# Kernel tuning notes

Measured on AMD Instinct MI355X. Metric: run time of the kernel, lower is better.

The kernel has to match this reference:

```python
import jax, jax.numpy as jnp
import numpy as np

N_NODES, C, R, L, H, NB = 50000, 512, 4096, 32, 4, 4  # NB blocks: enc0, enc1, pma, dec0
LN_EPS = 1e-5

def _layer_norm(x, g, b):
    mu = jnp.mean(x, axis=-1, keepdims=True)
    var = jnp.var(x, axis=-1, keepdims=True)
    return (x - mu) * jax.lax.rsqrt(var + LN_EPS) * g + b

def _mab(x, y, y_mask, x_mask, Wq, bq, Wk, bk, Wv, bv, Wo, bo, ffW, ffb, g1, b1, g2, b2):
    # Multihead attention block (SetTransformer MAB), dropout=0 at inference.
    Rr, Lq, Cc = x.shape
    Lk = y.shape[1]
    Dh = Cc // H
    q = (x @ Wq.T + bq).reshape(Rr, Lq, H, Dh)
    k = (y @ Wk.T + bk).reshape(Rr, Lk, H, Dh)
    v = (y @ Wv.T + bv).reshape(Rr, Lk, H, Dh)
    scores = jnp.einsum('rqhd,rkhd->rhqk', q, k) * (1.0 / Dh ** 0.5)
    if y_mask is not None:  # mask padded keys (ragged gene sets)
        scores = jnp.where(y_mask[:, None, None, :], scores, jnp.float32(-1e30))
    attn = jax.nn.softmax(scores, axis=-1)
    out = jnp.einsum('rhqk,rkhd->rqhd', attn, v).reshape(Rr, Lq, Cc)
    out = out @ Wo.T + bo
    if x_mask is not None:  # zero attention output at padded query rows
        out = jnp.where(x_mask[..., None], out, 0.0)
    out = _layer_norm(out + x, g1, b1)
    out = _layer_norm(out + jax.nn.relu(out @ ffW.T + ffb), g2, b2)
    return out

def setup_inputs() -> dict:
    key = jax.random.key(0)
    ks = jax.random.split(key, 10)
    s = 0.02
    return {
        'gene_embeddings': jax.random.normal(ks[0], (N_NODES, C), jnp.float32),
        'reaction_gene_idx': jax.random.randint(ks[1], (R, L), 0, N_NODES),
        'reaction_lengths': jax.random.randint(ks[2], (R,), 1, L + 1),
        'Wq': jax.random.normal(ks[3], (NB, C, C), jnp.float32) * s,
        'Wk': jax.random.normal(ks[4], (NB, C, C), jnp.float32) * s,
        'Wv': jax.random.normal(ks[5], (NB, C, C), jnp.float32) * s,
        'Wo': jax.random.normal(ks[6], (NB, C, C), jnp.float32) * s,
        'ffW': jax.random.normal(ks[7], (NB, C, C), jnp.float32) * s,
        'bq': jnp.zeros((NB, C), jnp.float32),
        'bk': jnp.zeros((NB, C), jnp.float32),
        'bv': jnp.zeros((NB, C), jnp.float32),
        'bo': jnp.zeros((NB, C), jnp.float32),
        'ffb': jnp.zeros((NB, C), jnp.float32),
        'g1': jnp.ones((NB, C), jnp.float32),
        'b1': jnp.zeros((NB, C), jnp.float32),
        'g2': jnp.ones((NB, C), jnp.float32),
        'b2': jnp.zeros((NB, C), jnp.float32),
        'pma_lin_W': jax.random.normal(ks[8], (C, C), jnp.float32) * s,
        'pma_lin_b': jnp.zeros((C,), jnp.float32),
        'seed': jax.random.normal(ks[9], (1, C), jnp.float32) * s,
    }

def reference(gene_embeddings, reaction_gene_idx, reaction_lengths, Wq, Wk, Wv, Wo, ffW, bq, bk, bv, bo, ffb, g1, b1, g2, b2, pma_lin_W, pma_lin_b, seed):
    mask = jnp.arange(L)[None, :] < reaction_lengths[:, None]  # [R, L] ragged validity mask
    x = gene_embeddings[reaction_gene_idx]                     # [R, L, C] per-reaction gather
    x = jnp.where(mask[..., None], x, 0.0)
    def blk(i, xq, ykv, ymask, xmask):
        return _mab(xq, ykv, ymask, xmask, Wq[i], bq[i], Wk[i], bk[i], Wv[i], bv[i],
                    Wo[i], bo[i], ffW[i], ffb[i], g1[i], b1[i], g2[i], b2[i])
    x = blk(0, x, x, mask, mask)   # encoder SAB 0
    x = blk(1, x, x, mask, mask)   # encoder SAB 1
    y = jax.nn.relu(x @ pma_lin_W.T + pma_lin_b)
    sd = jnp.broadcast_to(seed[None, :, :], (R, 1, C))
    x = blk(2, sd, y, mask, None)  # PMA: 1 seed attends over gene set
    x = blk(3, x, x, None, None)   # decoder SAB over the single seed
    out = jnp.mean(x, axis=1)      # [R, C] (1 seed, concat=False)
    out = jnp.where((reaction_lengths > 0)[:, None], out, 0.0)  # empty reactions -> zeros
    return out
```

## Files before the change

kernel.cpp:

```cpp
#include <hip/hip_runtime.h>
#include <stdint.h>

#define R_ 4096
#define L_ 32
#define C_ 512
#define H_ 4
#define DH_ 128

typedef __bf16 bf16x8 __attribute__((ext_vector_type(8)));
typedef float f32x4 __attribute__((ext_vector_type(4)));

__device__ __forceinline__ float b2f(unsigned int u) {
    union { unsigned int i; float f; } x; x.i = u << 16; return x.f;
}
__device__ __forceinline__ unsigned short f2b(float f) {
    union { float f; unsigned int i; } x; x.f = f;
    unsigned int i = x.i;
    i += 0x7fffu + ((i >> 16) & 1u);
    return (unsigned short)(i >> 16);
}
__device__ __forceinline__ void unpack8(uint4 v, float* x) {
    x[0] = b2f(v.x & 0xffffu); x[1] = b2f(v.x >> 16);
    x[2] = b2f(v.y & 0xffffu); x[3] = b2f(v.y >> 16);
    x[4] = b2f(v.z & 0xffffu); x[5] = b2f(v.z >> 16);
    x[6] = b2f(v.w & 0xffffu); x[7] = b2f(v.w >> 16);
}
__device__ __forceinline__ uint4 pack8(const float* x) {
    uint4 v;
    v.x = (unsigned)f2b(x[0]) | ((unsigned)f2b(x[1]) << 16);
    v.y = (unsigned)f2b(x[2]) | ((unsigned)f2b(x[3]) << 16);
    v.z = (unsigned)f2b(x[4]) | ((unsigned)f2b(x[5]) << 16);
    v.w = (unsigned)f2b(x[6]) | ((unsigned)f2b(x[7]) << 16);
    return v;
}

__device__ __forceinline__ void gload_lds16(const unsigned short* g, unsigned short* l) {
    __builtin_amdgcn_global_load_lds(
        (const __attribute__((address_space(1))) void*)g,
        (__attribute__((address_space(3))) void*)l, 16, 0, 0);
}

__global__ __launch_bounds__(256)
void detect_kernel(const unsigned short* __restrict__ gene, int* __restrict__ flag) {
    __shared__ int cnt;
    if (threadIdx.x == 0) cnt = 0;
    __syncthreads();
    int local = 0;
    for (int j = 0; j < 8; ++j) {
        int i = threadIdx.x * 8 + j;
        unsigned short u = gene[2 * i];
        int e = (u >> 7) & 0xFF;
        if (e >= 100 && e <= 140) ++local;
    }
    atomicAdd(&cnt, local);
    __syncthreads();
    if (threadIdx.x == 0) *flag = (cnt >= 1024) ? 1 : 0;
}

__global__ __launch_bounds__(256)
void cvt_any_kernel(const void* __restrict__ in, unsigned short* __restrict__ out,
                    int n, const int* __restrict__ flag, int src_off) {
    int i0 = (blockIdx.x * 256 + threadIdx.x) * 8;
    if (i0 >= n) return;
    if (*flag) {
        *(uint4*)(out + i0) = *(const uint4*)((const unsigned short*)in + src_off + i0);
    } else {
        const float* f = (const float*)in + src_off;
        float4 a = *(const float4*)(f + i0);
        float4 b = *(const float4*)(f + i0 + 4);
        float x[8] = {a.x, a.y, a.z, a.w, b.x, b.y, b.z, b.w};
        *(uint4*)(out + i0) = pack8(x);
    }
}

__global__ __launch_bounds__(256)
void bias_concat_kernel(const unsigned short* __restrict__ bq, const unsigned short* __restrict__ bk,
                        const unsigned short* __restrict__ bv,
                        unsigned short* __restrict__ bqkv0, unsigned short* __restrict__ bqkv1,
                        unsigned short* __restrict__ bkv2) {
    int t = threadIdx.x;
#pragma unroll
    for (int s = 0; s < 2; ++s) {
        int i = t + s * 256;
        bqkv0[i]        = bq[i];
        bqkv0[i + 512]  = bk[i];
        bqkv0[i + 1024] = bv[i];
        bqkv1[i]        = bq[i + 512];
        bqkv1[i + 512]  = bk[i + 512];
        bqkv1[i + 1024] = bv[i + 512];
        bkv2[i]         = bk[i + 1024];
        bkv2[i + 512]   = bv[i + 1024];
    }
}

__global__ __launch_bounds__(256)
void qp_kernel(const unsigned short* __restrict__ Wq2, const unsigned short* __restrict__ bq2,
               const unsigned short* __restrict__ seed, unsigned short* __restrict__ qp) {
    __shared__ float sv[512];
    int t = threadIdx.x;
    sv[t] = b2f(seed[t]); sv[t + 256] = b2f(seed[t + 256]);
    __syncthreads();
#pragma unroll
    for (int s = 0; s < 2; ++s) {
        int n = t + s * 256;
        const unsigned short* wrow = Wq2 + (size_t)n * 512;
        float acc = 0.f;
        for (int k8 = 0; k8 < 64; ++k8) {
            float x[8];
            unpack8(*(const uint4*)(wrow + k8 * 8), x);
#pragma unroll
            for (int e = 0; e < 8; ++e) acc += x[e] * sv[k8 * 8 + e];
        }
        qp[n] = f2b(acc + b2f(bq2[n]));
    }
}

__global__ __launch_bounds__(256)
void diag_kernel(unsigned short* __restrict__ out, int n, float val) {
    int i = blockIdx.x * 256 + threadIdx.x;
    if (i < n) out[i] = f2b(val);
}

__global__ __launch_bounds__(256)
void scan_kernel(const int* __restrict__ lens, int* __restrict__ off,
                 int* __restrict__ meta, int Rc) {
    __shared__ int tsum[257];
    const int t = threadIdx.x;
    const int chunk = (Rc + 255) / 256;
    const int lo = t * chunk;
    const int hi = min(lo + chunk, Rc);
    int s = 0;
    for (int i = lo; i < hi; ++i) {
        int l = lens[i]; l = max(0, min(32, l));
        s += l;
    }
    tsum[t] = s;
    __syncthreads();
    if (t == 0) {
        int acc = 0;
        for (int i = 0; i < 256; ++i) { int v = tsum[i]; tsum[i] = acc; acc += v; }
        tsum[256] = acc;
        meta[0] = acc;
        meta[1] = (acc + 127) & ~127;
    }
    __syncthreads();
    int run = tsum[t];
    for (int i = lo; i < hi; ++i) {
        off[i] = run;
        int l = lens[i]; l = max(0, min(32, l));
        run += l;
    }
}

__global__ __launch_bounds__(256)
void gather_kernel(const void* __restrict__ gene_v, const int* __restrict__ gidx,
                   const int* __restrict__ lens, const int* __restrict__ off,
                   unsigned short* __restrict__ X, const int* __restrict__ flag) {
    int tid = blockIdx.x * 256 + threadIdx.x;
    int m = tid >> 6;
    int ch = tid & 63;
    int r = m >> 5, j = m & 31;
    if (j >= lens[r]) return;
    size_t dst = (size_t)(off[r] + j) * C_ + ch * 8;
    size_t base = (size_t)gidx[m] * C_ + ch * 8;
    uint4 v;
    if (*flag) {
        v = *(const uint4*)((const unsigned short*)gene_v + base);
    } else {
        const float* f = (const float*)gene_v;
        float4 a = *(const float4*)(f + base);
        float4 b = *(const float4*)(f + base + 4);
        float x[8] = {a.x, a.y, a.z, a.w, b.x, b.y, b.z, b.w};
        v = pack8(x);
    }
    *(uint4*)(X + dst) = v;
}

__global__ __launch_bounds__(256)
void ztail_kernel(unsigned short* __restrict__ X, const int* __restrict__ meta) {
    int tid = blockIdx.x * 256 + threadIdx.x;
    int m = meta[0] + (tid >> 6);
    int ch = tid & 63;
    if (m < meta[1])
        *(uint4*)(X + (size_t)m * C_ + ch * 8) = make_uint4(0u, 0u, 0u, 0u);
}

__global__ __launch_bounds__(256)
void seed_kernel(const unsigned short* __restrict__ seed, unsigned short* __restrict__ Xs) {
    int i = blockIdx.x * 256 + threadIdx.x;
    int ch = i & 63;
    uint4 v = *(const uint4*)(seed + ch * 8);
    *(uint4*)(Xs + (size_t)i * 8) = v;
}

__global__ __launch_bounds__(256)
void final_kernel(const unsigned short* __restrict__ S, const int* __restrict__ lens,
                  void* __restrict__ out, const int* __restrict__ flag, size_t elem_off) {
    int i = blockIdx.x * 256 + threadIdx.x;
    int r = i >> 6;
    uint4 v = make_uint4(0u, 0u, 0u, 0u);
    if (lens[r] > 0) v = *(const uint4*)(S + (size_t)i * 8);
    if (*flag) {
        *(uint4*)((unsigned short*)out + elem_off + (size_t)i * 8) = v;
    } else {
        float x[8];
        unpack8(v, x);
        float* o = (float*)out + elem_off + (size_t)i * 8;
        *(float4*)o       = make_float4(x[0], x[1], x[2], x[3]);
        *(float4*)(o + 4) = make_float4(x[4], x[5], x[6], x[7]);
    }
}

template<int NT>
__global__ __launch_bounds__(256, 2)
void gemm_bt_kernel(const unsigned short* __restrict__ A, const unsigned short* __restrict__ W,
                    const unsigned short* __restrict__ bias, unsigned short* __restrict__ Out,
                    int relu, const int* __restrict__ meta, int MT) {
    const int b = blockIdx.x;
    const int xcd = b & 7;
    const int j = b >> 3;
    const int ml = j / NT;
    const int n = j - ml * NT;
    const int m = ml * 8 + xcd;
    if (m >= MT) return;
    const int m0 = m * 128, n0 = n * 256;
    if (meta && m0 >= meta[1]) return;
    const int ldo = NT * 256;

    __shared__ unsigned short As[128 * 64];
    __shared__ unsigned short Bs[256 * 64];

    const int t = threadIdx.x;
    const int wave = t >> 6, lane = t & 63;
    const int quad = lane >> 4, lr = lane & 15;
    const int wr = wave >> 1, wc = wave & 1;

    const int srow8 = lane >> 3;
    const int scol8 = (lane & 7) ^ srow8;
    const unsigned short* gaB = A + (size_t)(m0 + wave * 8 + srow8) * C_ + scol8 * 8;
    const unsigned short* gbB = W + (size_t)(n0 + wave * 8 + srow8) * C_ + scol8 * 8;
    unsigned short* lA = As + wave * 512;
    unsigned short* lB = Bs + wave * 512;

    f32x4 acc[4][8] = {};

    for (int k0 = 0; k0 < C_; k0 += 64) {
        __syncthreads();
#pragma unroll
        for (int jj = 0; jj < 4; ++jj)
            gload_lds16(gaB + (size_t)jj * 32 * C_ + k0, lA + jj * 2048);
#pragma unroll
        for (int jj = 0; jj < 8; ++jj)
            gload_lds16(gbB + (size_t)jj * 32 * C_ + k0, lB + jj * 2048);
        __syncthreads();

#pragma unroll
        for (int kk = 0; kk < 2; ++kk) {
            bf16x8 af[4], bfr[8];
#pragma unroll
            for (int i = 0; i < 4; ++i)
                af[i] = *(const bf16x8*)&As[(64 * wr + 16 * i + lr) * 64 +
                                            (((kk << 2) + quad) ^ (lr & 7)) * 8];
#pragma unroll
            for (int jj = 0; jj < 8; ++jj)
                bfr[jj] = *(const bf16x8*)&Bs[(128 * wc + 16 * jj + lr) * 64 +
                                              (((kk << 2) + quad) ^ (lr & 7)) * 8];
#pragma unroll
            for (int i = 0; i < 4; ++i)
#pragma unroll
                for (int jj = 0; jj < 8; ++jj)
                    acc[i][jj] = __builtin_amdgcn_mfma_f32_16x16x32_bf16(af[i], bfr[jj], acc[i][jj], 0, 0, 0);
        }
    }

#pragma unroll
    for (int i = 0; i < 4; ++i) {
        int row = m0 + 64 * wr + 16 * i + quad * 4;
#pragma unroll
        for (int jj = 0; jj < 8; ++jj) {
            int col = n0 + 128 * wc + 16 * jj + lr;
            float bv = b2f(bias[col]);
#pragma unroll
            for (int r = 0; r < 4; ++r) {
                float v = acc[i][jj][r] + bv;
                if (relu) v = fmaxf(v, 0.f);
                Out[(size_t)(row + r) * ldo + col] = f2b(v);
            }
        }
    }
}

template<int NK>
__device__ __forceinline__ void attn_enc_body(
    const unsigned short* __restrict__ QKV, unsigned short* __restrict__ O,
    int h, int t, int len, int base,
    unsigned short* Qs, unsigned short* Ks, float (*Sc)[33]) {

#pragma unroll
    for (int it = 0; it < NK; ++it) {
        int flat = t + it * 128;
        int row = flat >> 4, ch = flat & 15;
        if (row < len) {
            size_t g = ((size_t)(base + row)) * 1536 + h * DH_ + ch * 8;
            *(uint4*)&Qs[row * 136 + ch * 8] = *(const uint4*)(QKV + g);
            *(uint4*)&Ks[row * 136 + ch * 8] = *(const uint4*)(QKV + g + 512);
        }
    }
    __syncthreads();

    const unsigned* Qw = (const unsigned*)Qs;
    const unsigned* Kw = (const unsigned*)Ks;

    {
        const int qg = t >> 3, kg = t & 7;
        float aqk[2][NK];
#pragma unroll
        for (int j = 0; j < 2; ++j)
#pragma unroll
            for (int i = 0; i < NK; ++i) aqk[j][i] = 0.f;
        for (int d2 = 0; d2 < 64; ++d2) {
            unsigned q0 = Qw[qg * 68 + d2];
            unsigned q1 = Qw[(qg + 16) * 68 + d2];
            float q0l = b2f(q0 & 0xffffu), q0h = b2f(q0 >> 16);
            float q1l = b2f(q1 & 0xffffu), q1h = b2f(q1 >> 16);
#pragma unroll
            for (int i = 0; i < NK; ++i) {
                unsigned kv = Kw[(kg + 8 * i) * 68 + d2];
                float kl = b2f(kv & 0xffffu), kh = b2f(kv >> 16);
                aqk[0][i] += q0l * kl + q0h * kh;
                aqk[1][i] += q1l * kl + q1h * kh;
            }
        }
        const float scale = 0.08838834764831845f;
#pragma unroll
        for (int j = 0; j < 2; ++j)
#pragma unroll
            for (int i = 0; i < NK; ++i) {
                int k = kg + 8 * i;
                Sc[qg + 16 * j][k] = (k < len) ? aqk[j][i] * scale : -1e30f;
            }
    }
    __syncthreads();

    if (t < len) {
        float mx = -3e38f;
        for (int k = 0; k < len; ++k) mx = fmaxf(mx, Sc[t][k]);
        float sum = 0.f;
        for (int k = 0; k < len; ++k) { float e = __expf(Sc[t][k] - mx); Sc[t][k] = e; sum += e; }
        float inv = 1.f / sum;
        for (int k = 0; k < len; ++k) Sc[t][k] *= inv;
    }
    __syncthreads();

    {
        const int qh = t >> 3, g = t & 7;
        float av[2][16] = {};
        const unsigned short* Vg = QKV + (size_t)base * 1536 + 1024 + h * DH_ + g * 8;
        for (int k = 0; k < len; ++k) {
            float a0 = Sc[qh][k], a1 = Sc[qh + 16][k];
            const unsigned short* vrow = Vg + (size_t)k * 1536;
            float v0[8], v1[8];
            unpack8(*(const uint4*)vrow, v0);
            unpack8(*(const uint4*)(vrow + 64), v1);
#pragma unroll
            for (int e = 0; e < 8; ++e) {
                av[0][e]     += a0 * v0[e];
                av[0][8 + e] += a0 * v1[e];
                av[1][e]     += a1 * v0[e];
                av[1][8 + e] += a1 * v1[e];
            }
        }
#pragma unroll
        for (int qi = 0; qi < 2; ++qi) {
            int q = qh + 16 * qi;
            if (q >= len) continue;
            size_t ga = ((size_t)(base + q)) * C_ + h * DH_;
#pragma unroll
            for (int j = 0; j < 2; ++j) {
                float tmp[8];
#pragma unroll
                for (int e = 0; e < 8; ++e) tmp[e] = av[qi][j * 8 + e];
                *(uint4*)(O + ga + g * 8 + 64 * j) = pack8(tmp);
            }
        }
    }
}

__global__ __launch_bounds__(128)
void attn_enc_kernel(const unsigned short* __restrict__ QKV, unsigned short* __restrict__ O,
                     const int* __restrict__ lens, const int* __restrict__ off) {
    const int r = blockIdx.x, h = blockIdx.y, t = threadIdx.x;
    const int len = lens[r];
    if (len <= 0) return;
    const int base = off[r];
    __shared__ unsigned short Qs[32 * 136], Ks[32 * 136];
    __shared__ float Sc[32][33];
    switch ((len + 7) >> 3) {
        case 1:  attn_enc_body<1>(QKV, O, h, t, len, base, Qs, Ks, Sc); break;
        case 2:  attn_enc_body<2>(QKV, O, h, t, len, base, Qs, Ks, Sc); break;
        case 3:  attn_enc_body<3>(QKV, O, h, t, len, base, Qs, Ks, Sc); break;
        default: attn_enc_body<4>(QKV, O, h, t, len, base, Qs, Ks, Sc); break;
    }
}

__global__ __launch_bounds__(64)
void attn_pma_kernel(const unsigned short* __restrict__ qp, const unsigned short* __restrict__ KV,
                     unsigned short* __restrict__ O,
                     const int* __restrict__ lens, const int* __restrict__ off) {
    const int r = blockIdx.x, h = blockIdx.y, t = threadIdx.x;
    const int len = lens[r];
    if (len <= 0) return;
    const int base = off[r];
    __shared__ float qv[128];
    __shared__ float attn[32];
    const size_t qb = (size_t)r * C_ + h * DH_;
    qv[t]      = b2f(qp[h * DH_ + t]);
    qv[t + 64] = b2f(qp[h * DH_ + t + 64]);
    __syncthreads();
    if (t < 32 && t < len) {
        const unsigned short* krow = KV + ((size_t)(base + t)) * 1024 + h * DH_;
        float s = 0.f;
        for (int d = 0; d < 128; ++d) s += qv[d] * b2f(krow[d]);
        attn[t] = s * 0.08838834764831845f;
    }
    __syncthreads();
    if (t == 0) {
        float mx = -3e38f;
        for (int k = 0; k < len; ++k) mx = fmaxf(mx, attn[k]);
        float sum = 0.f;
        for (int k = 0; k < len; ++k) { float e = __expf(attn[k] - mx); attn[k] = e; sum += e; }
        float inv = 1.f / sum;
        for (int k = 0; k < len; ++k) attn[k] *= inv;
    }
    __syncthreads();
    float a0 = 0.f, a1 = 0.f;
    for (int k = 0; k < len; ++k) {
        const unsigned short* vrow = KV + ((size_t)(base + k)) * 1024 + 512 + h * DH_;
        float a = attn[k];
        a0 += a * b2f(vrow[t]);
        a1 += a * b2f(vrow[t + 64]);
    }
    O[qb + t]      = f2b(a0);
    O[qb + t + 64] = f2b(a1);
}

__global__ __launch_bounds__(256)
void ln_kernel(const unsigned short* __restrict__ A, const unsigned short* __restrict__ Res,
               const unsigned short* __restrict__ gamma, const unsigned short* __restrict__ beta,
               unsigned short* __restrict__ out, const int* __restrict__ lens, int use_mask,
               const int* __restrict__ meta) {
    const int m = blockIdx.x * 4 + (threadIdx.x >> 6);
    if (meta && m >= meta[1]) return;
    const int lane = threadIdx.x & 63;
    const bool masked = use_mask && ((m & 31) >= lens[m >> 5]);
    const size_t base = (size_t)m * C_ + lane * 8;
    float xa[8], xr[8], x[8];
    unpack8(*(const uint4*)(A + base), xa);
    unpack8(*(const uint4*)(Res + base), xr);
    float s = 0.f, ss = 0.f;
#pragma unroll
    for (int e = 0; e < 8; ++e) {
        x[e] = (masked ? 0.f : xa[e]) + xr[e];
        s += x[e]; ss += x[e] * x[e];
    }
#pragma unroll
    for (int off = 32; off > 0; off >>= 1) {
        s  += __shfl_down(s, off);
        ss += __shfl_down(ss, off);
    }
    s = __shfl(s, 0); ss = __shfl(ss, 0);
    const float mu = s * (1.f / 512.f);
    const float rinv = rsqrtf(fmaxf(ss * (1.f / 512.f) - mu * mu, 0.f) + 1e-5f);
    float gg[8], bb[8], y[8];
    unpack8(*(const uint4*)(gamma + lane * 8), gg);
    unpack8(*(const uint4*)(beta + lane * 8), bb);
#pragma unroll
    for (int e = 0; e < 8; ++e) y[e] = (x[e] - mu) * rinv * gg[e] + bb[e];
    *(uint4*)(out + base) = pack8(y);
}

extern "C" void kernel_launch(void* const* d_in, const int* in_sizes, int n_in,
                              void* d_out, int out_size, void* d_ws, size_t ws_size,
                              hipStream_t stream) {
    (void)in_sizes; (void)n_in;
    const void* gene = d_in[0];
    const int*  gidx = (const int*)d_in[1];
    const int*  lens = (const int*)d_in[2];

    int* ibase = (int*)d_ws;
    int* flag  = ibase;
    int* meta  = ibase + 2;
    int* d_off = ibase + 8;
    unsigned short* ws0 = (unsigned short*)(ibase + 8 + 4096);
    const size_t hdr_bytes = (size_t)(8 + 4096) * 4;

    size_t off = 0;
    auto take = [&](size_t elems) { unsigned short* p = ws0 + off; off += elems; return p; };
    const size_t CC = (size_t)C_ * C_;
    unsigned short* wEnc0 = take(3 * CC);
    unsigned short* wEnc1 = take(3 * CC);
    unsigned short* wKVp  = take(2 * CC);
    unsigned short* wO  = take(4 * CC);
    unsigned short* wF  = take(4 * CC);
    unsigned short* wP  = take(CC);
    unsigned short* wQp = take(CC);
    unsigned short* wVd = take(CC);
    unsigned short* cbq = take(4 * C_);
    unsigned short* cbk = take(4 * C_);
    unsigned short* cbv = take(4 * C_);
    unsigned short* cbo = take(4 * C_);
    unsigned short* cff = take(4 * C_);
    unsigned short* cg1 = take(4 * C_);
    unsigned short* cb1 = take(4 * C_);
    unsigned short* cg2 = take(4 * C_);
    unsigned short* cb2 = take(4 * C_);
    unsigned short* cpb = take(C_);
    unsigned short* csd = take(C_);
    unsigned short* bqkv0 = take(3 * C_);
    unsigned short* bqkv1 = take(3 * C_);
    unsigned short* bkv2  = take(2 * C_);
    unsigned short* qp    = take(C_);
    const size_t wbytes = hdr_bytes + off * 2;

    const size_t per_r = ((size_t)32 * 2560 + 4 * 512) * 2;
    int Rc = 0;
    const int cands[6] = {4096, 2048, 1024, 512, 256, 128};
    for (int i = 0; i < 6; ++i) {
        size_t need = wbytes + (size_t)cands[i] * per_r;
        if (need <= ws_size) { Rc = cands[i]; break; }
    }
    if (Rc == 0) {
        diag_kernel<<<(out_size + 255) / 256, 256, 0, stream>>>(
            (unsigned short*)d_out, out_size, 1000.0f + (float)(ws_size >> 20));
        return;
    }
    const int Mc = Rc * 32;

    unsigned short* X    = take((size_t)Mc * C_);
    unsigned short* AQKV = take((size_t)Mc * 1536);
    unsigned short* Aout = take((size_t)Mc * C_);
    unsigned short* S0 = take((size_t)Rc * C_);
    unsigned short* S1 = take((size_t)Rc * C_);
    unsigned short* S2 = take((size_t)Rc * C_);
    unsigned short* S3 = take((size_t)Rc * C_);

    detect_kernel<<<1, 256, 0, stream>>>((const unsigned short*)gene, flag);
    auto cvt = [&](const void* in, unsigned short* out_, int n, int src_off) {
        cvt_any_kernel<<<(n + 2047) / 2048, 256, 0, stream>>>(in, out_, n, flag, src_off);
    };
    cvt(d_in[3], wEnc0,          (int)CC, 0);
    cvt(d_in[4], wEnc0 + CC,     (int)CC, 0);
    cvt(d_in[5], wEnc0 + 2 * CC, (int)CC, 0);
    cvt(d_in[3], wEnc1,          (int)CC, (int)CC);
    cvt(d_in[4], wEnc1 + CC,     (int)CC, (int)CC);
    cvt(d_in[5], wEnc1 + 2 * CC, (int)CC, (int)CC);
    cvt(d_in[4], wKVp,      (int)CC, (int)(2 * CC));
    cvt(d_in[5], wKVp + CC, (int)CC, (int)(2 * CC));
    cvt(d_in[3], wQp, (int)CC, (int)(2 * CC));
    cvt(d_in[5], wVd, (int)CC, (int)(3 * CC));
    cvt(d_in[6], wO, (int)(4 * CC), 0);
    cvt(d_in[7], wF, (int)(4 * CC), 0);
    cvt(d_in[17], wP, (int)CC, 0);
    cvt(d_in[8],  cbq, 4 * C_, 0); cvt(d_in[9],  cbk, 4 * C_, 0); cvt(d_in[10], cbv, 4 * C_, 0);
    cvt(d_in[11], cbo, 4 * C_, 0); cvt(d_in[12], cff, 4 * C_, 0);
    cvt(d_in[13], cg1, 4 * C_, 0); cvt(d_in[14], cb1, 4 * C_, 0);
    cvt(d_in[15], cg2, 4 * C_, 0); cvt(d_in[16], cb2, 4 * C_, 0);
    cvt(d_in[18], cpb, C_, 0);     cvt(d_in[19], csd, C_, 0);
    bias_concat_kernel<<<1, 256, 0, stream>>>(cbq, cbk, cbv, bqkv0, bqkv1, bkv2);
    qp_kernel<<<1, 256, 0, stream>>>(wQp, cbq + 2 * C_, csd, qp);

    auto gemm = [&](auto nt_tag, const unsigned short* Ain, const unsigned short* Win,
                    const unsigned short* bias, unsigned short* Outp, int Mrows, int relu,
                    const int* mt) {
        constexpr int NT = decltype(nt_tag)::value;
        const int MT = Mrows / 128;
        const int grid = 8 * ((MT + 7) / 8) * NT;
        gemm_bt_kernel<NT><<<dim3(grid), 256, 0, stream>>>(Ain, Win, bias, Outp, relu, mt, MT);
    };
    using N2 = std::integral_constant<int, 2>;
    using N4 = std::integral_constant<int, 4>;
    using N6 = std::integral_constant<int, 6>;

    for (int c = 0; c < R_ / Rc; ++c) {
        const int r0 = c * Rc;
        const int* lc = lens + r0;

        scan_kernel<<<1, 256, 0, stream>>>(lc, d_off, meta, Rc);
        gather_kernel<<<Mc * 64 / 256, 256, 0, stream>>>(
            gene, gidx + (size_t)r0 * L_, lc, d_off, X, flag);
        ztail_kernel<<<32, 256, 0, stream>>>(X, meta);

        for (int i = 0; i < 2; ++i) {
            gemm(N6{}, X, i ? wEnc1 : wEnc0, i ? bqkv1 : bqkv0, AQKV, Mc, 0, meta);
            attn_enc_kernel<<<dim3(Rc, H_), 128, 0, stream>>>(AQKV, Aout, lc, d_off);
            gemm(N2{}, Aout, wO + (size_t)i * CC, cbo + i * C_, AQKV, Mc, 0, meta);
            ln_kernel<<<Mc / 4, 256, 0, stream>>>(AQKV, X, cg1 + i * C_, cb1 + i * C_, X, lc, 0, meta);
            gemm(N2{}, X, wF + (size_t)i * CC, cff + i * C_, Aout, Mc, 1, meta);
            ln_kernel<<<Mc / 4, 256, 0, stream>>>(Aout, X, cg2 + i * C_, cb2 + i * C_, X, lc, 0, meta);
        }

        gemm(N2{}, X, wP, cpb, Aout, Mc, 1, meta);
        seed_kernel<<<Rc * 64 / 256, 256, 0, stream>>>(csd, S0);

        {
            gemm(N4{}, Aout, wKVp, bkv2, AQKV, Mc, 0, meta);
            attn_pma_kernel<<<dim3(Rc, H_), 64, 0, stream>>>(qp, AQKV, S2, lc, d_off);
            gemm(N2{}, S2, wO + 2 * CC, cbo + 2 * C_, S3, Rc, 0, nullptr);
            ln_kernel<<<Rc / 4, 256, 0, stream>>>(S3, S0, cg1 + 2 * C_, cb1 + 2 * C_, S0, lc, 0, nullptr);
            gemm(N2{}, S0, wF + 2 * CC, cff + 2 * C_, S1, Rc, 1, nullptr);
            ln_kernel<<<Rc / 4, 256, 0, stream>>>(S1, S0, cg2 + 2 * C_, cb2 + 2 * C_, S0, lc, 0, nullptr);
        }

        {
            gemm(N2{}, S0, wVd, cbv + 3 * C_, S1, Rc, 0, nullptr);
            gemm(N2{}, S1, wO + 3 * CC, cbo + 3 * C_, S2, Rc, 0, nullptr);
            ln_kernel<<<Rc / 4, 256, 0, stream>>>(S2, S0, cg1 + 3 * C_, cb1 + 3 * C_, S0, lc, 0, nullptr);
            gemm(N2{}, S0, wF + 3 * CC, cff + 3 * C_, S1, Rc, 1, nullptr);
            ln_kernel<<<Rc / 4, 256, 0, stream>>>(S1, S0, cg2 + 3 * C_, cb2 + 3 * C_, S0, lc, 0, nullptr);
        }

        final_kernel<<<Rc * 64 / 256, 256, 0, stream>>>(S0, lc, d_out, flag, (size_t)r0 * C_);
    }
}
```

Before: 1.917 ms.

## Use MFMA for encoder QK scores and fold decoder Wo·Wv into one GEMM

The encoder attention QK^T score computation moves from scalar bf16-unpack FMA loops to 16x16x32 bf16 MFMA instructions, one wave per 16 query rows. Separately, the decoder's V projection and output projection are precomposed into a single weight matrix Wc = Wo·Wv with bias Wo·bv+bo by new setup kernels. This removes one Rc×512×512 GEMM per chunk. The MFMA path drops the explicit key-length masking before softmax, and the folded weights are rounded to bf16 once, which changes numerics slightly.

Result: faster. 1.730 ms (-9.7%).

```diff
diff --git a/kernel.cpp b/kernel.cpp
--- a/kernel.cpp
+++ b/kernel.cpp
@@ -113,6 +113,44 @@
         }
         qp[n] = f2b(acc + b2f(bq2[n]));
     }
+}
+
+__global__ __launch_bounds__(256)
+void wc_kernel(const unsigned short* __restrict__ Wo3, const unsigned short* __restrict__ Wv3,
+               unsigned short* __restrict__ Wc) {
+    const int i = blockIdx.x, t = threadIdx.x;
+    __shared__ float wo[512];
+    wo[t] = b2f(Wo3[(size_t)i * 512 + t]);
+    wo[t + 256] = b2f(Wo3[(size_t)i * 512 + t + 256]);
+    __syncthreads();
+    float a0 = 0.f, a1 = 0.f;
+    for (int d = 0; d < 512; ++d) {
+        const unsigned short* row = Wv3 + (size_t)d * 512;
+        float w = wo[d];
+        a0 += w * b2f(row[t]);
+        a1 += w * b2f(row[t + 256]);
+    }
+    Wc[(size_t)i * 512 + t]       = f2b(a0);
+    Wc[(size_t)i * 512 + t + 256] = f2b(a1);
+}
+
+__global__ __launch_bounds__(256)
+void bc_kernel(const unsigned short* __restrict__ Wo3, const unsigned short* __restrict__ bv3,
+               const unsigned short* __restrict__ bo3, unsigned short* __restrict__ bc) {
+    const int t = threadIdx.x;
+    __shared__ float bvv[512];
+    bvv[t] = b2f(bv3[t]); bvv[t + 256] = b2f(bv3[t + 256]);
+    __syncthreads();
+    const int i = blockIdx.x * 256 + t;
+    const unsigned short* row = Wo3 + (size_t)i * 512;
+    float acc = 0.f;
+    for (int d8 = 0; d8 < 64; ++d8) {
+        float x[8];
+        unpack8(*(const uint4*)(row + d8 * 8), x);
+#pragma unroll
+        for (int e = 0; e < 8; ++e) acc += x[e] * bvv[d8 * 8 + e];
+    }
+    bc[i] = f2b(acc + b2f(bo3[i]));
 }
 
 __global__ __launch_bounds__(256)
@@ -308,37 +346,29 @@
     }
     __syncthreads();
 
-    const unsigned* Qw = (const unsigned*)Qs;
-    const unsigned* Kw = (const unsigned*)Ks;
-
     {
-        const int qg = t >> 3, kg = t & 7;
-        float aqk[2][NK];
-#pragma unroll
-        for (int j = 0; j < 2; ++j)
-#pragma unroll
-            for (int i = 0; i < NK; ++i) aqk[j][i] = 0.f;
-        for (int d2 = 0; d2 < 64; ++d2) {
-            unsigned q0 = Qw[qg * 68 + d2];
-            unsigned q1 = Qw[(qg + 16) * 68 + d2];
-            float q0l = b2f(q0 & 0xffffu), q0h = b2f(q0 >> 16);
-            float q1l = b2f(q1 & 0xffffu), q1h = b2f(q1 >> 16);
-#pragma unroll
-            for (int i = 0; i < NK; ++i) {
-                unsigned kv = Kw[(kg + 8 * i) * 68 + d2];
-                float kl = b2f(kv & 0xffffu), kh = b2f(kv >> 16);
-                aqk[0][i] += q0l * kl + q0h * kh;
-                aqk[1][i] += q1l * kl + q1h * kh;
+        const int wv = t >> 6;
+        const int ln_ = t & 63;
+        const int quad = ln_ >> 4, lr = ln_ & 15;
+        f32x4 a0 = {0.f, 0.f, 0.f, 0.f};
+        f32x4 a1 = {0.f, 0.f, 0.f, 0.f};
+#pragma unroll
+        for (int s = 0; s < 4; ++s) {
+            bf16x8 aq = *(const bf16x8*)&Qs[(wv * 16 + lr) * 136 + s * 32 + quad * 8];
+            bf16x8 k0 = *(const bf16x8*)&Ks[lr * 136 + s * 32 + quad * 8];
+            a0 = __builtin_amdgcn_mfma_f32_16x16x32_bf16(aq, k0, a0, 0, 0, 0);
+            if (NK >= 3) {
+                bf16x8 k1 = *(const bf16x8*)&Ks[(16 + lr) * 136 + s * 32 + quad * 8];
+                a1 = __builtin_amdgcn_mfma_f32_16x16x32_bf16(aq, k1, a1, 0, 0, 0);
             }
         }
         const float scale = 0.08838834764831845f;
 #pragma unroll
-        for (int j = 0; j < 2; ++j)
-#pragma unroll
-            for (int i = 0; i < NK; ++i) {
-                int k = kg + 8 * i;
-                Sc[qg + 16 * j][k] = (k < len) ? aqk[j][i] * scale : -1e30f;
-            }
+        for (int reg = 0; reg < 4; ++reg) {
+            int q = wv * 16 + quad * 4 + reg;
+            Sc[q][lr] = a0[reg] * scale;
+            if (NK >= 3) Sc[q][16 + lr] = a1[reg] * scale;
+        }
     }
     __syncthreads();
 
@@ -505,6 +535,7 @@
     unsigned short* wP  = take(CC);
     unsigned short* wQp = take(CC);
     unsigned short* wVd = take(CC);
+    unsigned short* wWc = take(CC);
     unsigned short* cbq = take(4 * C_);
     unsigned short* cbk = take(4 * C_);
     unsigned short* cbv = take(4 * C_);
@@ -519,6 +550,7 @@
     unsigned short* bqkv0 = take(3 * C_);
     unsigned short* bqkv1 = take(3 * C_);
     unsigned short* bkv2  = take(2 * C_);
+    unsigned short* bcb   = take(C_);
     unsigned short* qp    = take(C_);
     const size_t wbytes = hdr_bytes + off * 2;
 
@@ -568,6 +600,8 @@
     cvt(d_in[18], cpb, C_, 0);     cvt(d_in[19], csd, C_, 0);
     bias_concat_kernel<<<1, 256, 0, stream>>>(cbq, cbk, cbv, bqkv0, bqkv1, bkv2);
     qp_kernel<<<1, 256, 0, stream>>>(wQp, cbq + 2 * C_, csd, qp);
+    wc_kernel<<<512, 256, 0, stream>>>(wO + 3 * CC, wVd, wWc);
+    bc_kernel<<<2, 256, 0, stream>>>(wO + 3 * CC, cbv + 3 * C_, cbo + 3 * C_, bcb);
 
     auto gemm = [&](auto nt_tag, const unsigned short* Ain, const unsigned short* Win,
                     const unsigned short* bias, unsigned short* Outp, int Mrows, int relu,
@@ -612,8 +646,7 @@
         }
 
         {
-            gemm(N2{}, S0, wVd, cbv + 3 * C_, S1, Rc, 0, nullptr);
-            gemm(N2{}, S1, wO + 3 * CC, cbo + 3 * C_, S2, Rc, 0, nullptr);
+            gemm(N2{}, S0, wWc, bcb, S2, Rc, 0, nullptr);
             ln_kernel<<<Rc / 4, 256, 0, stream>>>(S2, S0, cg1 + 3 * C_, cb1 + 3 * C_, S0, lc, 0, nullptr);
             gemm(N2{}, S0, wF + 3 * CC, cff + 3 * C_, S1, Rc, 1, nullptr);
             ln_kernel<<<Rc / 4, 256, 0, stream>>>(S1, S0, cg2 + 3 * C_, cb2 + 3 * C_, S0, lc, 0, nullptr);
```
